# Optimization experiments

Measured on AMD Instinct MI355X. Metric: run time of the kernel, lower is better.

Reference implementation:

```python
import jax, jax.numpy as jnp
import numpy as np

jax.config.update("jax_enable_x64", True)

# Dims (see shape_source): batch, heads, q-len, kv-len, head-channels, quant group
B, H, T, S, HC = 2, 16, 1024, 1024, 128
G = 8            # group_size from A/R_QUANT_PARAMS
SCALE_SHIFT = 14 # combined dequant shift applied to integer QK scores before softmax
O_SM = 14        # fixed-point offset of the integer softmax output (LUT-style)
PROB_QMAX = 255.0  # 8-bit unsigned probability mantissa (R_QUANT_PARAMS n_bits=8)


def _dequant_po2(q, s):
    """q: int mantissas [..., N], s: nonneg po2 shift exponents [..., N//G].
    Emulates (q << s) per group of G channels (pot_scale activation quantizer)."""
    s_full = jnp.repeat(s, G, axis=-1)
    return q.astype(jnp.float64) * jnp.exp2(s_full.astype(jnp.float64))


def setup_inputs() -> dict:
    key = jax.random.key(0)
    ks = jax.random.split(key, 6)
    # signed 8-bit mantissas in [-128, 127]
    q_q = jax.random.randint(ks[0], (B, H, T, HC), 0, 256, dtype=jnp.int32) - 128
    k_q = jax.random.randint(ks[1], (B, H, S, HC), 0, 256, dtype=jnp.int32) - 128
    vt_q = jax.random.randint(ks[2], (B, H, HC, S), 0, 256, dtype=jnp.int32) - 128
    # nonnegative power-of-two shifts, one per group of G=8
    q_s = jax.random.randint(ks[3], (B, H, T, HC // G), 0, 4, dtype=jnp.int32)
    k_s = jax.random.randint(ks[4], (B, H, S, HC // G), 0, 4, dtype=jnp.int32)
    vt_s = jax.random.randint(ks[5], (B, H, HC, S // G), 0, 4, dtype=jnp.int32)
    return {"q_q": q_q, "q_s": q_s, "k_q": k_q, "k_s": k_s, "vt_q": vt_q, "vt_s": vt_s}


def reference(q_q, q_s, k_q, k_s, vt_q, vt_s):
    # ---- shift_qk_matmul: (q_q << q_s) @ (k_q << k_s)^T in float64, truncated to int64
    q = _dequant_po2(q_q, q_s)                       # [B,H,T,HC] f64
    k = _dequant_po2(k_q, k_s)                       # [B,H,S,HC] f64
    scores = jnp.einsum("bhtc,bhsc->bhts", q, k).astype(jnp.int64)

    # ---- integer softmax emulation: rescale integer scores, softmax, then
    # re-quantize probabilities with an 8-bit per-group (G=8 along S) po2 scale
    logits = scores.astype(jnp.float32) * np.float32(2.0 ** (-SCALE_SHIFT) / np.sqrt(HC))
    p = jax.nn.softmax(logits, axis=-1)              # [B,H,T,S]
    val = jnp.round(p * (2.0 ** O_SM))               # fixed-point probs (ints)
    vg = val.reshape(B, H, T, S // G, G)
    gmax = jnp.max(vg, axis=-1, keepdims=True)
    r_shift = jnp.clip(jnp.ceil(jnp.log2(jnp.maximum(gmax, 1.0) / PROB_QMAX)), 0.0, None)
    r_q = jnp.clip(jnp.round(vg / jnp.exp2(r_shift)), 0.0, PROB_QMAX)
    r = (r_q * jnp.exp2(r_shift)).reshape(B, H, T, S).astype(jnp.float64)  # (r_q << r_s)

    # ---- shift_rv_matmul: r @ (vt_q << vt_s)^T in float64, truncated to int64
    vt = _dequant_po2(vt_q, vt_s)                    # [B,H,HC,S] f64
    a = jnp.einsum("bhts,bhcs->bhtc", r, vt).astype(jnp.int64)  # [B,H,T,HC]
    return a
```

## Files before the change

kernel.cpp:

```cpp
#include <hip/hip_runtime.h>


typedef int v4i __attribute__((ext_vector_type(4)));

#define BHN 32
#define TN  1024
#define SN  1024
#define HCN 128
#define TT  16
#define RST 1032
#define WS_NEED (2u*8388608u)

__device__ __forceinline__ unsigned pack_b(int b0,int b1,int b2,int b3){
    return (unsigned)((b0&255)|((b1&255)<<8)|((b2&255)<<16)|((b3&255)<<24));
}

__device__ __forceinline__ void dig16(const int* __restrict__ p, int s0, int s1,
                                      v4i& hi, v4i& lo){
    #pragma unroll
    for (int wi=0; wi<4; ++wi){
        v4i m = *(const v4i*)(p + wi*4);
        int s = (wi<2) ? s0 : s1;
        int d0=m[0]<<s, d1=m[1]<<s, d2=m[2]<<s, d3=m[3]<<s;
        hi[wi] = (int)pack_b(d0>>4,d1>>4,d2>>4,d3>>4);
        lo[wi] = (int)pack_b(d0&15,d1&15,d2&15,d3&15);
    }
}

__global__ __launch_bounds__(256) void digitize(
    const int* __restrict__ k_q, const int* __restrict__ k_s,
    const int* __restrict__ vt_q, const int* __restrict__ vt_s,
    unsigned char* __restrict__ kd, unsigned char* __restrict__ vd)
{
    const int g = blockIdx.x*256 + threadIdx.x;
    const int ioff = g*16;
    if (blockIdx.y == 0){
        int row = ioff>>7, c0 = ioff&127;
        int s0 = k_s[(row<<4)+(c0>>3)], s1 = k_s[(row<<4)+(c0>>3)+1];
        v4i hi, lo;
        dig16(k_q + ioff, s0, s1, hi, lo);
        int bh = row>>10, srow = row&1023;
        int ch = srow>>7, lr = srow&127, n = lr>>4, ln = lr&15;
        int kc = c0>>6, q4 = (c0>>4)&3;
        size_t base = (size_t)(bh*8+ch)*32768u
                    + (size_t)(n*4096 + kc*2048 + (q4*16+ln)*16);
        *(v4i*)(kd + base)        = hi;
        *(v4i*)(kd + base + 1024) = lo;
    } else {
        int grow = ioff>>10, s4 = ioff&1023;
        int s0 = vt_s[(grow<<7)+(s4>>3)], s1 = vt_s[(grow<<7)+(s4>>3)+1];
        v4i hi, lo;
        dig16(vt_q + ioff, s0, s1, hi, lo);
        int bh = grow>>7, chan = grow&127;
        int ch = s4>>7, sl = s4&127;
        int n = chan>>4, ln = chan&15;
        int kc = sl>>6, q4 = (sl>>4)&3;
        size_t base = (size_t)(bh*8+ch)*32768u
                    + (size_t)(n*4096 + kc*2048 + (q4*16+ln)*16);
        *(v4i*)(vd + base)        = hi;
        *(v4i*)(vd + base + 1024) = lo;
    }
}

template<bool PK>
__global__ __launch_bounds__(256,4) void mha_mfma(
    const int* __restrict__ q_q, const int* __restrict__ q_s,
    const int* __restrict__ k_q, const int* __restrict__ k_s,
    const int* __restrict__ vt_q, const int* __restrict__ vt_s,
    const unsigned char* __restrict__ kd, const unsigned char* __restrict__ vd,
    int* __restrict__ out)
{
    __shared__ unsigned short rbuf[16*RST];
    __shared__ float red[128];

    const int tid  = threadIdx.x;
    const int ln   = tid & 15;
    const int qd4  = (tid >> 4) & 3;
    const int w    = tid >> 6;
    const int lane = tid & 63;
    const int blk = blockIdx.x;
    const int bh  = ((blk>>9)<<3) | (blk&7);
    const int t0  = ((blk>>3)&63) * TT;

    v4i qfh[2], qfl[2];
    {
        const int* qrow  = q_q + (size_t)(bh*TN + t0 + ln)*HCN;
        const int* qsrow = q_s + (size_t)(bh*TN + t0 + ln)*16;
        #pragma unroll
        for (int kc=0; kc<2; ++kc){
            int gi = kc*8 + qd4*2;
            dig16(qrow + kc*64 + qd4*16, qsrow[gi], qsrow[gi+1], qfh[kc], qfl[kc]);
        }
    }

    int scv[16][4];

    const v4i* kb = (const v4i*)(kd + (size_t)bh*262144u);
    for (int ch=0; ch<8; ++ch){
        #pragma unroll
        for (int i=0;i<2;i++){
            const int n = w*2 + i;
            v4i a2{0,0,0,0}, a1{0,0,0,0}, a0{0,0,0,0};
            #pragma unroll
            for (int kc=0;kc<2;kc++){
                v4i bhv, blv;
                if (PK){
                    const v4i* tb = kb + (ch*8+n)*256 + kc*128 + lane;
                    bhv = tb[0];
                    blv = tb[64];
                } else {
                    int srow = bh*SN + ch*128 + n*16 + ln;
                    int cc   = kc*64 + qd4*16;
                    dig16(k_q + (size_t)srow*128 + cc,
                          k_s[srow*16 + (cc>>3)], k_s[srow*16 + (cc>>3) + 1], bhv, blv);
                }
                a2 = __builtin_amdgcn_mfma_i32_16x16x64_i8(qfh[kc], bhv, a2, 0,0,0);
                a1 = __builtin_amdgcn_mfma_i32_16x16x64_i8(qfl[kc], bhv, a1, 0,0,0);
                a1 = __builtin_amdgcn_mfma_i32_16x16x64_i8(qfh[kc], blv, a1, 0,0,0);
                a0 = __builtin_amdgcn_mfma_i32_16x16x64_i8(qfl[kc], blv, a0, 0,0,0);
            }
            int st = ch*2 + i;
            #pragma unroll
            for (int r=0;r<4;r++)
                scv[st][r] = (a2[r]<<8) + (a1[r]<<4) + a0[r];
        }
    }

    const float CS = (float)(6.103515625e-05 / 11.313708498984760390566);
    float mx[4], sm[4];
    #pragma unroll
    for (int r=0;r<4;r++){
        float m_ = -3.0e38f;
        #pragma unroll
        for (int st=0;st<16;st++) m_ = fmaxf(m_, (float)scv[st][r]*CS);
        #pragma unroll
        for (int o=8;o>0;o>>=1) m_ = fmaxf(m_, __shfl_xor(m_, o));
        mx[r] = m_;
    }
    if (ln == 0){
        #pragma unroll
        for (int r=0;r<4;r++) red[w*16 + qd4*4 + r] = mx[r];
    }
    __syncthreads();
    #pragma unroll
    for (int r=0;r<4;r++){
        float m_ = fmaxf(fmaxf(red[qd4*4+r], red[16+qd4*4+r]),
                         fmaxf(red[32+qd4*4+r], red[48+qd4*4+r]));
        float s_ = 0.f;
        #pragma unroll
        for (int st=0;st<16;st++){
            float e = expf((float)scv[st][r]*CS - m_);
            scv[st][r] = __float_as_int(e);
            s_ += e;
        }
        #pragma unroll
        for (int o=8;o>0;o>>=1) s_ += __shfl_xor(s_, o);
        sm[r] = s_;
    }
    if (ln == 0){
        #pragma unroll
        for (int r=0;r<4;r++) red[64 + w*16 + qd4*4 + r] = sm[r];
    }
    __syncthreads();
    float inv14[4];
    #pragma unroll
    for (int r=0;r<4;r++){
        float s_ = red[64+qd4*4+r] + red[80+qd4*4+r] + red[96+qd4*4+r] + red[112+qd4*4+r];
        inv14[r] = 16384.0f / s_;
    }

    #pragma unroll
    for (int st=0;st<16;st++){
        int colb = (st>>1)*128 + (w*2+(st&1))*16;
        #pragma unroll
        for (int r=0;r<4;r++){
            float val = rintf(__int_as_float(scv[st][r]) * inv14[r]);
            float g = val;
            g = fmaxf(g, __shfl_xor(g, 1));
            g = fmaxf(g, __shfl_xor(g, 2));
            g = fmaxf(g, __shfl_xor(g, 4));
            int gi = max((int)g, 1);
            int x = gi - 1;
            int e = 31 - __clz(x | 255);
            int sh = (e - 7) + ((x >> (e - 7)) == 255);
            float rq = fminf(rintf(val * __int_as_float((127-sh)<<23)), 255.0f);
            int rv = ((int)rq) << sh;
            int row = qd4*4 + r;
            int col = colb + ln;
            int gs  = (col>>3) ^ (row&7);
            rbuf[row*RST + gs*8 + (col&7)] = (unsigned short)rv;
        }
    }
    __syncthreads();

    const v4i* vb = (const v4i*)(vd + (size_t)bh*262144u);
    v4i acc[2][4];
    #pragma unroll
    for (int i=0;i<2;i++){
        #pragma unroll
        for (int j=0;j<4;j++) acc[i][j] = v4i{0,0,0,0};
    }
    for (int ch=0; ch<8; ++ch){
        #pragma unroll
        for (int kc=0;kc<2;kc++){
            int cb = ch*128 + kc*64 + qd4*16;
            int gg = cb>>3;
            const unsigned short* rp = rbuf + ln*RST;
            v4i r01 = *(const v4i*)(rp + ((gg    ^ (ln&7))<<3));
            v4i r23 = *(const v4i*)(rp + (((gg+1)^ (ln&7))<<3));
            unsigned u0=(unsigned)r01[0], u1=(unsigned)r01[1],
                     u2=(unsigned)r01[2], u3=(unsigned)r01[3],
                     u4=(unsigned)r23[0], u5=(unsigned)r23[1],
                     u6=(unsigned)r23[2], u7=(unsigned)r23[3];
            v4i rlv, rhv;
            rlv[0] = (int)__builtin_amdgcn_perm(u1, u0, 0x06040200u);
            rlv[1] = (int)__builtin_amdgcn_perm(u3, u2, 0x06040200u);
            rlv[2] = (int)__builtin_amdgcn_perm(u5, u4, 0x06040200u);
            rlv[3] = (int)__builtin_amdgcn_perm(u7, u6, 0x06040200u);
            rhv[0] = (int)__builtin_amdgcn_perm(u1+0x00800080u, u0+0x00800080u, 0x07050301u);
            rhv[1] = (int)__builtin_amdgcn_perm(u3+0x00800080u, u2+0x00800080u, 0x07050301u);
            rhv[2] = (int)__builtin_amdgcn_perm(u5+0x00800080u, u4+0x00800080u, 0x07050301u);
            rhv[3] = (int)__builtin_amdgcn_perm(u7+0x00800080u, u6+0x00800080u, 0x07050301u);
            #pragma unroll
            for (int i=0;i<2;i++){
                const int n = w*2 + i;
                v4i vh, vl;
                if (PK){
                    const v4i* tb = vb + (ch*8+n)*256 + kc*128 + lane;
                    vh = tb[0];
                    vl = tb[64];
                } else {
                    int chan = n*16 + ln;
                    int ss   = ch*128 + kc*64 + qd4*16;
                    dig16(vt_q + (size_t)(bh*HCN + chan)*SN + ss,
                          vt_s[(bh*HCN + chan)*128 + (ss>>3)],
                          vt_s[(bh*HCN + chan)*128 + (ss>>3) + 1], vh, vl);
                }
                acc[i][0] = __builtin_amdgcn_mfma_i32_16x16x64_i8(rhv, vh, acc[i][0], 0,0,0);
                acc[i][1] = __builtin_amdgcn_mfma_i32_16x16x64_i8(rhv, vl, acc[i][1], 0,0,0);
                acc[i][2] = __builtin_amdgcn_mfma_i32_16x16x64_i8(rlv, vh, acc[i][2], 0,0,0);
                acc[i][3] = __builtin_amdgcn_mfma_i32_16x16x64_i8(rlv, vl, acc[i][3], 0,0,0);
            }
        }
    }
    #pragma unroll
    for (int i=0;i<2;i++){
        #pragma unroll
        for (int r=0;r<4;r++){
            int o = (acc[i][0][r]<<12) + (acc[i][1][r]<<8) + (acc[i][2][r]<<4) + acc[i][3][r];
            out[(size_t)(bh*TN + t0 + qd4*4 + r)*HCN + (w*2+i)*16 + ln] = o;
        }
    }
}

extern "C" void kernel_launch(void* const* d_in, const int* in_sizes, int n_in,
                              void* d_out, int out_size, void* d_ws, size_t ws_size,
                              hipStream_t stream) {
    const int* q_q  = (const int*)d_in[0];
    const int* q_s  = (const int*)d_in[1];
    const int* k_q  = (const int*)d_in[2];
    const int* k_s  = (const int*)d_in[3];
    const int* vt_q = (const int*)d_in[4];
    const int* vt_s = (const int*)d_in[5];
    int* out = (int*)d_out;

    unsigned char* kd = (unsigned char*)d_ws;
    unsigned char* vd = kd + 8388608;

    if (ws_size >= (size_t)WS_NEED){
        digitize<<<dim3(1024,2), 256, 0, stream>>>(k_q,k_s,vt_q,vt_s, kd,vd);
        mha_mfma<true><<<dim3(2048), 256, 0, stream>>>(
            q_q,q_s,k_q,k_s,vt_q,vt_s, kd,vd, out);
    } else {
        mha_mfma<false><<<dim3(2048), 256, 0, stream>>>(
            q_q,q_s,k_q,k_s,vt_q,vt_s, kd,vd, out);
    }
}
```

Measured before the change: 174.1 us.

## Use Karatsuba for QK int8 split and bf16 MFMA for RV matmul

The QK integer matmul now uses a Karatsuba-style trick: a precomputed hi+lo digit sum replaces the two cross-term MFMAs, so three int8 MFMAs run instead of four. This costs a third packed K buffer in the workspace and an extra register array for Q. The RV matmul drops the four-way nibble decomposition and instead converts the probabilities and the shifted V values to bf16, using one bf16 MFMA per tile with float accumulation and rounding at the end. This cuts MFMA count and the perm unpacking, but it depends on the bf16 values and float sums staying exact. With 8-bit mantissas times power-of-two shifts and a 1024-long sum that could lose exactness against the int64 reference.

```diff
diff --git a/kernel.cpp b/kernel.cpp
--- a/kernel.cpp
+++ b/kernel.cpp
@@ -1,7 +1,10 @@
 #include <hip/hip_runtime.h>
-
-
-typedef int v4i __attribute__((ext_vector_type(4)));
+#include <string.h>
+
+
+typedef int   v4i __attribute__((ext_vector_type(4)));
+typedef float v4f __attribute__((ext_vector_type(4)));
+typedef short v8s __attribute__((ext_vector_type(8)));
 
 #define BHN 32
 #define TN  1024
@@ -9,22 +12,31 @@
 #define HCN 128
 #define TT  16
 #define RST 1032
-#define WS_NEED (2u*8388608u)
+#define KD_BH 393216
+#define VD_BH 262144
+#define WS_NEED ((size_t)BHN*(KD_BH+VD_BH))
 
 __device__ __forceinline__ unsigned pack_b(int b0,int b1,int b2,int b3){
     return (unsigned)((b0&255)|((b1&255)<<8)|((b2&255)<<16)|((b3&255)<<24));
 }
 
-__device__ __forceinline__ void dig16(const int* __restrict__ p, int s0, int s1,
-                                      v4i& hi, v4i& lo){
+__device__ __forceinline__ void dig16s(const int* __restrict__ p, int s0, int s1,
+                                       v4i& hi, v4i& lo, v4i& sm){
     #pragma unroll
     for (int wi=0; wi<4; ++wi){
         v4i m = *(const v4i*)(p + wi*4);
         int s = (wi<2) ? s0 : s1;
         int d0=m[0]<<s, d1=m[1]<<s, d2=m[2]<<s, d3=m[3]<<s;
-        hi[wi] = (int)pack_b(d0>>4,d1>>4,d2>>4,d3>>4);
-        lo[wi] = (int)pack_b(d0&15,d1&15,d2&15,d3&15);
-    }
+        int h0=d0>>4, h1=d1>>4, h2=d2>>4, h3=d3>>4;
+        int l0=d0&15, l1=d1&15, l2=d2&15, l3=d3&15;
+        hi[wi] = (int)pack_b(h0,h1,h2,h3);
+        lo[wi] = (int)pack_b(l0,l1,l2,l3);
+        sm[wi] = (int)pack_b(h0+l0,h1+l1,h2+l2,h3+l3);
+    }
+}
+
+__device__ __forceinline__ unsigned short bf16_of_int(int v){
+    return (unsigned short)(__float_as_uint((float)v) >> 16);
 }
 
 __global__ __launch_bounds__(256) void digitize(
@@ -37,28 +49,37 @@
     if (blockIdx.y == 0){
         int row = ioff>>7, c0 = ioff&127;
         int s0 = k_s[(row<<4)+(c0>>3)], s1 = k_s[(row<<4)+(c0>>3)+1];
-        v4i hi, lo;
-        dig16(k_q + ioff, s0, s1, hi, lo);
+        v4i hi, lo, sm;
+        dig16s(k_q + ioff, s0, s1, hi, lo, sm);
         int bh = row>>10, srow = row&1023;
-        int ch = srow>>7, lr = srow&127, n = lr>>4, ln = lr&15;
+        int ch = srow>>7, lr = srow&127, n = lr>>4, l15 = lr&15;
         int kc = c0>>6, q4 = (c0>>4)&3;
-        size_t base = (size_t)(bh*8+ch)*32768u
-                    + (size_t)(n*4096 + kc*2048 + (q4*16+ln)*16);
+        size_t base = (size_t)bh*KD_BH + (size_t)ch*49152u
+                    + (size_t)(((n*2+kc)*3)*1024 + (q4*16+l15)*16);
         *(v4i*)(kd + base)        = hi;
         *(v4i*)(kd + base + 1024) = lo;
+        *(v4i*)(kd + base + 2048) = sm;
     } else {
         int grow = ioff>>10, s4 = ioff&1023;
-        int s0 = vt_s[(grow<<7)+(s4>>3)], s1 = vt_s[(grow<<7)+(s4>>3)+1];
-        v4i hi, lo;
-        dig16(vt_q + ioff, s0, s1, hi, lo);
+        int sc0 = vt_s[(grow<<7)+(s4>>3)], sc1 = vt_s[(grow<<7)+(s4>>3)+1];
         int bh = grow>>7, chan = grow&127;
-        int ch = s4>>7, sl = s4&127;
-        int n = chan>>4, ln = chan&15;
-        int kc = sl>>6, q4 = (sl>>4)&3;
-        size_t base = (size_t)(bh*8+ch)*32768u
-                    + (size_t)(n*4096 + kc*2048 + (q4*16+ln)*16);
-        *(v4i*)(vd + base)        = hi;
-        *(v4i*)(vd + base + 1024) = lo;
+        int n = chan>>4, l15 = chan&15;
+        int kb = s4>>5, q0 = (s4>>3)&3;
+        const int* vp = vt_q + ioff;
+        #pragma unroll
+        for (int h=0; h<2; ++h){
+            int s = (h==0) ? sc0 : sc1;
+            unsigned wds[4];
+            #pragma unroll
+            for (int j=0; j<4; ++j){
+                int a = vp[h*8 + j*2]   << s;
+                int b = vp[h*8 + j*2+1] << s;
+                wds[j] = (unsigned)bf16_of_int(a) | ((unsigned)bf16_of_int(b) << 16);
+            }
+            size_t base = (size_t)bh*VD_BH
+                        + (size_t)(((kb*8 + n)*64 + (q0+h)*16 + l15)*16);
+            *(v4i*)(vd + base) = v4i{(int)wds[0],(int)wds[1],(int)wds[2],(int)wds[3]};
+        }
     }
 }
 
@@ -82,47 +103,50 @@
     const int bh  = ((blk>>9)<<3) | (blk&7);
     const int t0  = ((blk>>3)&63) * TT;
 
-    v4i qfh[2], qfl[2];
+    v4i qfh[2], qfl[2], qfs[2];
     {
         const int* qrow  = q_q + (size_t)(bh*TN + t0 + ln)*HCN;
         const int* qsrow = q_s + (size_t)(bh*TN + t0 + ln)*16;
         #pragma unroll
         for (int kc=0; kc<2; ++kc){
             int gi = kc*8 + qd4*2;
-            dig16(qrow + kc*64 + qd4*16, qsrow[gi], qsrow[gi+1], qfh[kc], qfl[kc]);
+            dig16s(qrow + kc*64 + qd4*16, qsrow[gi], qsrow[gi+1],
+                   qfh[kc], qfl[kc], qfs[kc]);
         }
     }
 
     int scv[16][4];
 
-    const v4i* kb = (const v4i*)(kd + (size_t)bh*262144u);
+    const v4i* kb_ = (const v4i*)(kd + (size_t)bh*KD_BH);
+    #pragma unroll 2
     for (int ch=0; ch<8; ++ch){
         #pragma unroll
         for (int i=0;i<2;i++){
             const int n = w*2 + i;
-            v4i a2{0,0,0,0}, a1{0,0,0,0}, a0{0,0,0,0};
+            v4i ahh{0,0,0,0}, ap3{0,0,0,0}, all{0,0,0,0};
             #pragma unroll
             for (int kc=0;kc<2;kc++){
-                v4i bhv, blv;
+                v4i kh, kl, ks;
                 if (PK){
-                    const v4i* tb = kb + (ch*8+n)*256 + kc*128 + lane;
-                    bhv = tb[0];
-                    blv = tb[64];
+                    const v4i* tb = kb_ + ch*3072 + (n*2+kc)*192 + lane;
+                    kh = tb[0]; kl = tb[64]; ks = tb[128];
                 } else {
                     int srow = bh*SN + ch*128 + n*16 + ln;
                     int cc   = kc*64 + qd4*16;
-                    dig16(k_q + (size_t)srow*128 + cc,
-                          k_s[srow*16 + (cc>>3)], k_s[srow*16 + (cc>>3) + 1], bhv, blv);
+                    dig16s(k_q + (size_t)srow*128 + cc,
+                           k_s[srow*16 + (cc>>3)], k_s[srow*16 + (cc>>3) + 1],
+                           kh, kl, ks);
                 }
-                a2 = __builtin_amdgcn_mfma_i32_16x16x64_i8(qfh[kc], bhv, a2, 0,0,0);
-                a1 = __builtin_amdgcn_mfma_i32_16x16x64_i8(qfl[kc], bhv, a1, 0,0,0);
-                a1 = __builtin_amdgcn_mfma_i32_16x16x64_i8(qfh[kc], blv, a1, 0,0,0);
-                a0 = __builtin_amdgcn_mfma_i32_16x16x64_i8(qfl[kc], blv, a0, 0,0,0);
+                ahh = __builtin_amdgcn_mfma_i32_16x16x64_i8(qfh[kc], kh, ahh, 0,0,0);
+                ap3 = __builtin_amdgcn_mfma_i32_16x16x64_i8(qfs[kc], ks, ap3, 0,0,0);
+                all = __builtin_amdgcn_mfma_i32_16x16x64_i8(qfl[kc], kl, all, 0,0,0);
             }
             int st = ch*2 + i;
             #pragma unroll
-            for (int r=0;r<4;r++)
-                scv[st][r] = (a2[r]<<8) + (a1[r]<<4) + a0[r];
+            for (int r=0;r<4;r++){
+                int mid = ap3[r] - ahh[r] - all[r];
+                scv[st][r] = (ahh[r]<<8) + (mid<<4) + all[r];
+            }
         }
     }
 
@@ -188,68 +212,48 @@
             int row = qd4*4 + r;
             int col = colb + ln;
             int gs  = (col>>3) ^ (row&7);
-            rbuf[row*RST + gs*8 + (col&7)] = (unsigned short)rv;
+            rbuf[row*RST + gs*8 + (col&7)] = bf16_of_int(rv);
         }
     }
     __syncthreads();
 
-    const v4i* vb = (const v4i*)(vd + (size_t)bh*262144u);
-    v4i acc[2][4];
-    #pragma unroll
-    for (int i=0;i<2;i++){
-        #pragma unroll
-        for (int j=0;j<4;j++) acc[i][j] = v4i{0,0,0,0};
-    }
-    for (int ch=0; ch<8; ++ch){
-        #pragma unroll
-        for (int kc=0;kc<2;kc++){
-            int cb = ch*128 + kc*64 + qd4*16;
-            int gg = cb>>3;
-            const unsigned short* rp = rbuf + ln*RST;
-            v4i r01 = *(const v4i*)(rp + ((gg    ^ (ln&7))<<3));
-            v4i r23 = *(const v4i*)(rp + (((gg+1)^ (ln&7))<<3));
-            unsigned u0=(unsigned)r01[0], u1=(unsigned)r01[1],
-                     u2=(unsigned)r01[2], u3=(unsigned)r01[3],
-                     u4=(unsigned)r23[0], u5=(unsigned)r23[1],
-                     u6=(unsigned)r23[2], u7=(unsigned)r23[3];
-            v4i rlv, rhv;
-            rlv[0] = (int)__builtin_amdgcn_perm(u1, u0, 0x06040200u);
-            rlv[1] = (int)__builtin_amdgcn_perm(u3, u2, 0x06040200u);
-            rlv[2] = (int)__builtin_amdgcn_perm(u5, u4, 0x06040200u);
-            rlv[3] = (int)__builtin_amdgcn_perm(u7, u6, 0x06040200u);
-            rhv[0] = (int)__builtin_amdgcn_perm(u1+0x00800080u, u0+0x00800080u, 0x07050301u);
-            rhv[1] = (int)__builtin_amdgcn_perm(u3+0x00800080u, u2+0x00800080u, 0x07050301u);
-            rhv[2] = (int)__builtin_amdgcn_perm(u5+0x00800080u, u4+0x00800080u, 0x07050301u);
-            rhv[3] = (int)__builtin_amdgcn_perm(u7+0x00800080u, u6+0x00800080u, 0x07050301u);
+    const v4i* vb = (const v4i*)(vd + (size_t)bh*VD_BH);
+    v4f acc0{0,0,0,0}, acc1{0,0,0,0};
+    #pragma unroll 4
+    for (int kb=0; kb<32; ++kb){
+        v8s af = *(const v8s*)(rbuf + ln*RST + (((kb*4+qd4) ^ (ln&7))<<3));
+        v4i b0, b1;
+        if (PK){
+            b0 = vb[(kb*8 + w*2    )*64 + lane];
+            b1 = vb[(kb*8 + w*2 + 1)*64 + lane];
+        } else {
             #pragma unroll
             for (int i=0;i<2;i++){
-                const int n = w*2 + i;
-                v4i vh, vl;
-                if (PK){
-                    const v4i* tb = vb + (ch*8+n)*256 + kc*128 + lane;
-                    vh = tb[0];
-                    vl = tb[64];
-                } else {
-                    int chan = n*16 + ln;
-                    int ss   = ch*128 + kc*64 + qd4*16;
-                    dig16(vt_q + (size_t)(bh*HCN + chan)*SN + ss,
-                          vt_s[(bh*HCN + chan)*128 + (ss>>3)],
-                          vt_s[(bh*HCN + chan)*128 + (ss>>3) + 1], vh, vl);
+                int chan = (w*2+i)*16 + ln;
+                const int* vp = vt_q + (size_t)(bh*HCN + chan)*SN + kb*32 + qd4*8;
+                int s = vt_s[(bh*HCN + chan)*128 + kb*4 + qd4];
+                unsigned wd[4];
+                #pragma unroll
+                for (int j=0;j<4;j++){
+                    int a = vp[j*2]   << s;
+                    int b = vp[j*2+1] << s;
+                    wd[j] = (unsigned)bf16_of_int(a) | ((unsigned)bf16_of_int(b)<<16);
                 }
-                acc[i][0] = __builtin_amdgcn_mfma_i32_16x16x64_i8(rhv, vh, acc[i][0], 0,0,0);
-                acc[i][1] = __builtin_amdgcn_mfma_i32_16x16x64_i8(rhv, vl, acc[i][1], 0,0,0);
-                acc[i][2] = __builtin_amdgcn_mfma_i32_16x16x64_i8(rlv, vh, acc[i][2], 0,0,0);
-                acc[i][3] = __builtin_amdgcn_mfma_i32_16x16x64_i8(rlv, vl, acc[i][3], 0,0,0);
-            }
-        }
-    }
-    #pragma unroll
-    for (int i=0;i<2;i++){
-        #pragma unroll
-        for (int r=0;r<4;r++){
-            int o = (acc[i][0][r]<<12) + (acc[i][1][r]<<8) + (acc[i][2][r]<<4) + acc[i][3][r];
-            out[(size_t)(bh*TN + t0 + qd4*4 + r)*HCN + (w*2+i)*16 + ln] = o;
-        }
+                v4i t{(int)wd[0],(int)wd[1],(int)wd[2],(int)wd[3]};
+                if (i==0) b0 = t; else b1 = t;
+            }
+        }
+        v8s bs0, bs1;
+        memcpy(&bs0, &b0, 16);
+        memcpy(&bs1, &b1, 16);
+        acc0 = __builtin_amdgcn_mfma_f32_16x16x32_bf16(af, bs0, acc0, 0,0,0);
+        acc1 = __builtin_amdgcn_mfma_f32_16x16x32_bf16(af, bs1, acc1, 0,0,0);
+    }
+    #pragma unroll
+    for (int r=0;r<4;r++){
+        size_t o = (size_t)(bh*TN + t0 + qd4*4 + r)*HCN + (w*2)*16 + ln;
+        out[o]      = (int)rintf(acc0[r]);
+        out[o + 16] = (int)rintf(acc1[r]);
     }
 }
 
@@ -265,9 +269,9 @@
     int* out = (int*)d_out;
 
     unsigned char* kd = (unsigned char*)d_ws;
-    unsigned char* vd = kd + 8388608;
-
-    if (ws_size >= (size_t)WS_NEED){
+    unsigned char* vd = kd + (size_t)BHN*KD_BH;
+
+    if (ws_size >= WS_NEED){
         digitize<<<dim3(1024,2), 256, 0, stream>>>(k_q,k_s,vt_q,vt_s, kd,vd);
         mha_mfma<true><<<dim3(2048), 256, 0, stream>>>(
             q_q,q_s,k_q,k_s,vt_q,vt_s, kd,vd, out);
```

Result: slower. 248.1 us (+42.5%).
